# Kernel tuning notes

Measured on AMD Instinct MI355X. Metric: run time of the kernel, lower is better.

Reference implementation:

```python
import jax, jax.numpy as jnp
import numpy as np

TOKENS, HIDDEN, FFN = 4096, 4096, 14336
SCALE = 0.02  # keep activations in a sane range


def setup_inputs() -> dict:
    key = jax.random.key(0)
    k1, k2, k3, k4 = jax.random.split(key, 4)
    x = jax.random.normal(k1, (TOKENS, HIDDEN), dtype=jnp.float32)
    expert_w1 = jax.random.normal(k2, (FFN, HIDDEN), dtype=jnp.float32) * SCALE
    expert_v1 = jax.random.normal(k3, (FFN, HIDDEN), dtype=jnp.float32) * SCALE
    expert_w2 = jax.random.normal(k4, (FFN, HIDDEN), dtype=jnp.float32) * SCALE
    return {"x": x, "expert_w1": expert_w1, "expert_v1": expert_v1, "expert_w2": expert_w2}


def reference(x, expert_w1, expert_v1, expert_w2):
    # gate/up projections: [T, H] @ [H, F] -> [T, F]
    gate = jnp.einsum('th,fh->tf', x, expert_w1)
    up = jnp.einsum('th,fh->tf', x, expert_v1)
    inter = jax.nn.silu(gate) * up            # fused SwiGLU intermediate [T, F]
    down = jnp.einsum('tf,fh->th', inter, expert_w2)  # [T, H]
    return down
```

## Files before the change

### kernel.cpp

```cpp
#include <hip/hip_runtime.h>
#include <hip/hip_bf16.h>
#include <stdint.h>

#define TOKENS 4096
#define HIDDEN 4096
#define FFN    14336

typedef __attribute__((ext_vector_type(8))) short bf16x8;
typedef __attribute__((ext_vector_type(4))) float f32x4;
typedef __attribute__((ext_vector_type(8))) unsigned short u16x8;

typedef __attribute__((address_space(3))) void lds_void_t;
typedef const __attribute__((address_space(1))) void gbl_void_t;

static __device__ __forceinline__ unsigned short f2b(float f) {
  union { float f; unsigned int u; } v; v.f = f;
  unsigned int u = v.u;
  return (unsigned short)((u + 0x7FFFu + ((u >> 16) & 1u)) >> 16);
}

__global__ void cvt_kernel(const float* __restrict__ in, unsigned short* __restrict__ out, long n) {
  long idx = (long)blockIdx.x * blockDim.x + threadIdx.x;
  long stride = (long)gridDim.x * blockDim.x;
  for (long i = idx * 4; i < n; i += stride * 4) {
    const float4 v = *reinterpret_cast<const float4*>(in + i);
    ushort4 o;
    o.x = f2b(v.x); o.y = f2b(v.y); o.z = f2b(v.z); o.w = f2b(v.w);
    *reinterpret_cast<ushort4*>(out + i) = o;
  }
}

__global__ void transpose_cvt_kernel(const float* __restrict__ in, unsigned short* __restrict__ out) {
  __shared__ float tile[64][65];
  const int f0 = blockIdx.x * 64;
  const int h0 = blockIdx.y * 64;
  const int t = threadIdx.x;
  const int rcol = (t & 15) * 4;
  const int rrow = t >> 4;
#pragma unroll
  for (int it = 0; it < 4; ++it) {
    int r = rrow + it * 16;
    const float4 v = *reinterpret_cast<const float4*>(in + (long)(f0 + r) * HIDDEN + h0 + rcol);
    tile[r][rcol] = v.x; tile[r][rcol + 1] = v.y; tile[r][rcol + 2] = v.z; tile[r][rcol + 3] = v.w;
  }
  __syncthreads();
  const int wrow = t >> 2;
  const int wc = (t & 3) * 16;
  u16x8 lo, hi;
#pragma unroll
  for (int j = 0; j < 8; ++j) lo[j] = f2b(tile[wc + j][wrow]);
#pragma unroll
  for (int j = 0; j < 8; ++j) hi[j] = f2b(tile[wc + 8 + j][wrow]);
  u16x8* dst = reinterpret_cast<u16x8*>(out + (long)(h0 + wrow) * FFN + f0 + wc);
  dst[0] = lo; dst[1] = hi;
}

#define MFMA16(a, b, c) __builtin_amdgcn_mfma_f32_16x16x32_bf16((a), (b), (c), 0, 0, 0)
#define SBAR()  __builtin_amdgcn_s_barrier()

static __device__ __forceinline__ int xcd_chunk(int bid, int nwg) {
  return (bid & 7) * (nwg >> 3) + (bid >> 3);
}

__global__ __launch_bounds__(512, 2)
void gateup256p_kernel(const unsigned short* __restrict__ X,
                       const unsigned short* __restrict__ W1,
                       const unsigned short* __restrict__ V1,
                       unsigned short* __restrict__ Inter) {
  __shared__ unsigned short sh[65536];
  const int tid = threadIdx.x, lane = tid & 63, wid = tid >> 6;
  const int wm = wid >> 2, wn = wid & 3;
  const int p = blockIdx.x;
  const int bm = p & 15;
  const int bnl = p >> 4;
  const int sr = tid >> 3;
  const int scb = (((tid & 7) ^ (sr & 7)) << 4);
  const int l15 = lane & 15;
  const int cb0 = (((lane >> 4) * 16) ^ ((lane & 7) << 4));
  const int cb1 = ((64 + (lane >> 4) * 16) ^ ((lane & 7) << 4));

  const unsigned short* Ap = X + (long)(bm * 256) * HIDDEN;

  auto LDA8 = [&](bf16x8* a, int buf, int cb) {
    const char* base = (const char*)sh + buf * 65536 + wm * 16384 + l15 * 128 + cb;
#pragma unroll
    for (int m = 0; m < 8; ++m) a[m] = *(const bf16x8*)(base + m * 2048);
  };
  auto LDW2 = [&](bf16x8* w, int buf, int cb) {
    const char* base = (const char*)sh + buf * 65536 + 32768 + (wn * 32 + l15) * 128 + cb;
    w[0] = *(const bf16x8*)(base);
    w[1] = *(const bf16x8*)(base + 2048);
  };
  auto LDV2 = [&](bf16x8* v, int buf, int cb) {
    const char* base = (const char*)sh + buf * 65536 + 49152 + (wn * 32 + l15) * 128 + cb;
    v[0] = *(const bf16x8*)(base);
    v[1] = *(const bf16x8*)(base + 2048);
  };

  for (int j = 0; j < 7; ++j) {
    const int bn = j * 16 + bnl;
    const unsigned short* Wp = W1 + (long)(bn * 128) * HIDDEN;
    const unsigned short* Vp = V1 + (long)(bn * 128) * HIDDEN;

    auto STA = [&](int u, int buf, int t) {
      const unsigned short* src = Ap + (long)(u * 64 + sr) * HIDDEN + t * 64 + (scb >> 1);
      unsigned short* dst = sh + buf * 32768 + u * 4096 + tid * 8;
      __builtin_amdgcn_global_load_lds((gbl_void_t*)src, (lds_void_t*)dst, 16, 0, 0);
    };
    auto STW = [&](int u, int buf, int t) {
      const unsigned short* src = Wp + (long)(u * 64 + sr) * HIDDEN + t * 64 + (scb >> 1);
      unsigned short* dst = sh + buf * 32768 + 16384 + u * 4096 + tid * 8;
      __builtin_amdgcn_global_load_lds((gbl_void_t*)src, (lds_void_t*)dst, 16, 0, 0);
    };
    auto STV = [&](int u, int buf, int t) {
      const unsigned short* src = Vp + (long)(u * 64 + sr) * HIDDEN + t * 64 + (scb >> 1);
      unsigned short* dst = sh + buf * 32768 + 24576 + u * 4096 + tid * 8;
      __builtin_amdgcn_global_load_lds((gbl_void_t*)src, (lds_void_t*)dst, 16, 0, 0);
    };

    f32x4 accg[8][2] = {};
    f32x4 accu[8][2] = {};

    STA(0, 0, 0); STA(1, 0, 0); STA(2, 0, 0); STA(3, 0, 0);
    STW(0, 0, 0); STW(1, 0, 0); STV(0, 0, 0); STV(1, 0, 0);

    bf16x8 a[8], w[2], v[2];
    const int NT = HIDDEN / 64;
    for (int t = 0; t < NT; ++t) {
      const int cur = t & 1, nxt = cur ^ 1;
      const bool pre = (t + 1 < NT);
      if (pre) { STW(0, nxt, t + 1); STW(1, nxt, t + 1);
                 STV(0, nxt, t + 1); STV(1, nxt, t + 1);
                 asm volatile("s_waitcnt vmcnt(4)" ::: "memory"); }
      else     { asm volatile("s_waitcnt vmcnt(0)" ::: "memory"); }
      SBAR();
      LDA8(a, cur, cb0); LDW2(w, cur, cb0);
      __builtin_amdgcn_s_setprio(1);
#pragma unroll
      for (int m = 0; m < 8; ++m) {
        accg[m][0] = MFMA16(a[m], w[0], accg[m][0]);
        accg[m][1] = MFMA16(a[m], w[1], accg[m][1]);
      }
      __builtin_amdgcn_s_setprio(0);
      SBAR();
      if (pre) { STA(0, nxt, t + 1); STA(1, nxt, t + 1);
                 STA(2, nxt, t + 1); STA(3, nxt, t + 1); }
      LDV2(v, cur, cb0);
      __builtin_amdgcn_s_setprio(1);
#pragma unroll
      for (int m = 0; m < 8; ++m) {
        accu[m][0] = MFMA16(a[m], v[0], accu[m][0]);
        accu[m][1] = MFMA16(a[m], v[1], accu[m][1]);
      }
      __builtin_amdgcn_s_setprio(0);
      SBAR();
      LDA8(a, cur, cb1); LDW2(w, cur, cb1);
      __builtin_amdgcn_s_setprio(1);
#pragma unroll
      for (int m = 0; m < 8; ++m) {
        accg[m][0] = MFMA16(a[m], w[0], accg[m][0]);
        accg[m][1] = MFMA16(a[m], w[1], accg[m][1]);
      }
      __builtin_amdgcn_s_setprio(0);
      SBAR();
      LDV2(v, cur, cb1);
      __builtin_amdgcn_s_setprio(1);
#pragma unroll
      for (int m = 0; m < 8; ++m) {
        accu[m][0] = MFMA16(a[m], v[0], accu[m][0]);
        accu[m][1] = MFMA16(a[m], v[1], accu[m][1]);
      }
      __builtin_amdgcn_s_setprio(0);
      SBAR();
    }
    const int r0 = (lane >> 4) * 4;
#pragma unroll
    for (int m = 0; m < 8; ++m)
#pragma unroll
      for (int n = 0; n < 2; ++n)
#pragma unroll
        for (int r = 0; r < 4; ++r) {
          const float g = accg[m][n][r];
          const float u = accu[m][n][r];
          const float s = g / (1.0f + __expf(-g));
          const int row = bm * 256 + wm * 128 + m * 16 + r0 + r;
          const int col = bn * 128 + wn * 32 + n * 16 + l15;
          Inter[(long)row * FFN + col] = f2b(s * u);
        }
    asm volatile("s_waitcnt vmcnt(0)" ::: "memory");
  }
}

__global__ __launch_bounds__(512, 2)
void down256_kernel(const unsigned short* __restrict__ Inter,
                    const unsigned short* __restrict__ W2t,
                    float* __restrict__ Out) {
  __shared__ unsigned short sh[65536];
  const int tid = threadIdx.x, lane = tid & 63, wid = tid >> 6;
  const int wm = wid >> 2, wn = wid & 3;
  const int swz = xcd_chunk(blockIdx.x, (TOKENS / 256) * (HIDDEN / 256));
  const int bm = swz & 15;
  const int bn = swz >> 4;
  const int sr = tid >> 3;
  const int scb = (((tid & 7) ^ (sr & 7)) << 4);
  const int l15 = lane & 15;
  const int cb0 = (((lane >> 4) * 16) ^ ((lane & 7) << 4));
  const int cb1 = ((64 + (lane >> 4) * 16) ^ ((lane & 7) << 4));

  const unsigned short* Ap = Inter + (long)(bm * 256) * FFN;
  const unsigned short* Bp = W2t + (long)(bn * 256) * FFN;

  f32x4 acc[8][4] = {};

  auto STAGE = [&](int kind, int h, int buf, int t) {
    const unsigned short* src = (kind ? Bp : Ap) + (long)(h * 128 + sr) * FFN + t * 64 + (scb >> 1);
    unsigned short* dst = sh + buf * 32768 + kind * 16384 + h * 8192 + tid * 8;
    __builtin_amdgcn_global_load_lds((gbl_void_t*)src, (lds_void_t*)dst, 16, 0, 0);
    __builtin_amdgcn_global_load_lds((gbl_void_t*)(src + 64L * FFN), (lds_void_t*)(dst + 4096), 16, 0, 0);
  };
  auto LDA8 = [&](bf16x8* a, int buf, int cb) {
    const char* base = (const char*)sh + buf * 65536 + wm * 16384 + l15 * 128 + cb;
#pragma unroll
    for (int m = 0; m < 8; ++m) a[m] = *(const bf16x8*)(base + m * 2048);
  };
  auto LDB2 = [&](bf16x8* b, int buf, int cb, int np) {
    const char* base = (const char*)sh + buf * 65536 + 32768 + (wn >> 1) * 16384 +
                       ((wn & 1) * 64 + l15) * 128 + cb;
    b[2 * np]     = *(const bf16x8*)(base + (2 * np) * 2048);
    b[2 * np + 1] = *(const bf16x8*)(base + (2 * np + 1) * 2048);
  };

  STAGE(0, 0, 0, 0); STAGE(0, 1, 0, 0); STAGE(1, 0, 0, 0); STAGE(1, 1, 0, 0);

  bf16x8 a[8], b[4];
  const int NT = FFN / 64;
  for (int t = 0; t < NT; ++t) {
    const int cur = t & 1, nxt = cur ^ 1;
    const bool pre = (t + 1 < NT);
    if (pre) { STAGE(1, 0, nxt, t + 1); STAGE(1, 1, nxt, t + 1);
               asm volatile("s_waitcnt vmcnt(4)" ::: "memory"); }
    else     { asm volatile("s_waitcnt vmcnt(0)" ::: "memory"); }
    SBAR();
    LDA8(a, cur, cb0); LDB2(b, cur, cb0, 0);
    __builtin_amdgcn_s_setprio(1);
#pragma unroll
    for (int m = 0; m < 8; ++m) {
      acc[m][0] = MFMA16(a[m], b[0], acc[m][0]);
      acc[m][1] = MFMA16(a[m], b[1], acc[m][1]);
    }
    __builtin_amdgcn_s_setprio(0);
    SBAR();
    if (pre) { STAGE(0, 0, nxt, t + 1); STAGE(0, 1, nxt, t + 1); }
    LDB2(b, cur, cb0, 1);
    __builtin_amdgcn_s_setprio(1);
#pragma unroll
    for (int m = 0; m < 8; ++m) {
      acc[m][2] = MFMA16(a[m], b[2], acc[m][2]);
      acc[m][3] = MFMA16(a[m], b[3], acc[m][3]);
    }
    __builtin_amdgcn_s_setprio(0);
    SBAR();
    LDA8(a, cur, cb1); LDB2(b, cur, cb1, 0);
    __builtin_amdgcn_s_setprio(1);
#pragma unroll
    for (int m = 0; m < 8; ++m) {
      acc[m][0] = MFMA16(a[m], b[0], acc[m][0]);
      acc[m][1] = MFMA16(a[m], b[1], acc[m][1]);
    }
    __builtin_amdgcn_s_setprio(0);
    SBAR();
    LDB2(b, cur, cb1, 1);
    __builtin_amdgcn_s_setprio(1);
#pragma unroll
    for (int m = 0; m < 8; ++m) {
      acc[m][2] = MFMA16(a[m], b[2], acc[m][2]);
      acc[m][3] = MFMA16(a[m], b[3], acc[m][3]);
    }
    __builtin_amdgcn_s_setprio(0);
    SBAR();
  }
  const int r0 = (lane >> 4) * 4;
#pragma unroll
  for (int m = 0; m < 8; ++m)
#pragma unroll
    for (int n = 0; n < 4; ++n)
#pragma unroll
      for (int r = 0; r < 4; ++r) {
        const int row = bm * 256 + wm * 128 + m * 16 + r0 + r;
        const int col = bn * 256 + wn * 64 + n * 16 + l15;
        Out[(long)row * HIDDEN + col] = acc[m][n][r];
      }
}

__device__ __forceinline__ void stage_tile_128(const unsigned short* __restrict__ g, long ldk,
                                               unsigned short* lds, int wave, int lane) {
#pragma unroll
  for (int it = 0; it < 2; ++it) {
    const int row = (it * 4 + wave) * 16 + (lane >> 2);
    const int kcol = (lane & 3) * 8;
    const unsigned short* src = g + (long)row * ldk + kcol;
    unsigned short* dst = lds + row * 32 + kcol;
    __builtin_amdgcn_global_load_lds((gbl_void_t*)src, (lds_void_t*)dst, 16, 0, 0);
  }
}

__global__ __launch_bounds__(256, 2)
void down_nt_kernel(const unsigned short* __restrict__ Inter,
                    const float* __restrict__ W2,
                    float* __restrict__ Out) {
  __shared__ unsigned short As[128 * 32];
  __shared__ unsigned short Bs[128 * 32];
  const int t = threadIdx.x;
  const int lane = t & 63;
  const int wave = t >> 6;
  const int bm = blockIdx.x & 31;
  const int bn = blockIdx.x >> 5;
  const int wm = (wave >> 1) * 64;
  const int wn = (wave & 1) * 64;
  const unsigned short* gA = Inter + (long)(bm * 128) * FFN;

  f32x4 acc[4][4] = {};
  const int fr = lane & 15;
  const int kg = (lane >> 4) * 8;
  const int p = lane & 15;
  const int h0 = wave * 32 + (lane >> 4) * 8;
  const float* gB = W2 + bn * 128 + h0;

  for (int kt = 0; kt < FFN; kt += 32) {
    __syncthreads();
    stage_tile_128(gA + kt, FFN, As, wave, lane);
    const float* r0p = gB + (long)(kt + 2 * p) * HIDDEN;
    const float* r1p = r0p + HIDDEN;
    const float4 a0 = *reinterpret_cast<const float4*>(r0p);
    const float4 a1 = *reinterpret_cast<const float4*>(r0p + 4);
    const float4 b0 = *reinterpret_cast<const float4*>(r1p);
    const float4 b1 = *reinterpret_cast<const float4*>(r1p + 4);
    unsigned short lo[8], hi[8];
    lo[0] = f2b(a0.x); lo[1] = f2b(a0.y); lo[2] = f2b(a0.z); lo[3] = f2b(a0.w);
    lo[4] = f2b(a1.x); lo[5] = f2b(a1.y); lo[6] = f2b(a1.z); lo[7] = f2b(a1.w);
    hi[0] = f2b(b0.x); hi[1] = f2b(b0.y); hi[2] = f2b(b0.z); hi[3] = f2b(b0.w);
    hi[4] = f2b(b1.x); hi[5] = f2b(b1.y); hi[6] = f2b(b1.z); hi[7] = f2b(b1.w);
#pragma unroll
    for (int j = 0; j < 8; ++j) {
      const unsigned int pack = (unsigned int)lo[j] | ((unsigned int)hi[j] << 16);
      *reinterpret_cast<unsigned int*>(&Bs[(h0 + j) * 32 + 2 * p]) = pack;
    }
    __syncthreads();
    bf16x8 a[4], b[4];
#pragma unroll
    for (int m = 0; m < 4; ++m)
      a[m] = *reinterpret_cast<const bf16x8*>(&As[(wm + m * 16 + fr) * 32 + kg]);
#pragma unroll
    for (int n = 0; n < 4; ++n)
      b[n] = *reinterpret_cast<const bf16x8*>(&Bs[(wn + n * 16 + fr) * 32 + kg]);
#pragma unroll
    for (int m = 0; m < 4; ++m)
#pragma unroll
      for (int n = 0; n < 4; ++n)
        acc[m][n] = MFMA16(a[m], b[n], acc[m][n]);
  }
  const int r0 = (lane >> 4) * 4;
#pragma unroll
  for (int m = 0; m < 4; ++m)
#pragma unroll
    for (int n = 0; n < 4; ++n)
#pragma unroll
      for (int r = 0; r < 4; ++r) {
        const int row = bm * 128 + wm + m * 16 + r0 + r;
        const int col = bn * 128 + wn + n * 16 + fr;
        Out[(long)row * HIDDEN + col] = acc[m][n][r];
      }
}

extern "C" void kernel_launch(void* const* d_in, const int* in_sizes, int n_in,
                              void* d_out, int out_size, void* d_ws, size_t ws_size,
                              hipStream_t stream) {
  const float* x  = (const float*)d_in[0];
  const float* w1 = (const float*)d_in[1];
  const float* v1 = (const float*)d_in[2];
  const float* w2 = (const float*)d_in[3];
  float* out = (float*)d_out;

  const size_t REQ_SMALL = 385875968UL;
  const size_t REQ_FULL  = 503316480UL;
  if (ws_size < REQ_SMALL) return;
  const bool full = (ws_size >= REQ_FULL);
  char* ws = (char*)d_ws;
  unsigned short* xb     = (unsigned short*)(ws);
  unsigned short* w1b    = (unsigned short*)(ws + 33554432L);
  unsigned short* v1b    = (unsigned short*)(ws + 150994944L);
  unsigned short* interb = (unsigned short*)(ws + 268435456L);
  unsigned short* w2tb   = (unsigned short*)(ws + 385875968L);

  hipLaunchKernelGGL(cvt_kernel, dim3(2048), dim3(256), 0, stream, x,  xb,  (long)TOKENS * HIDDEN);
  hipLaunchKernelGGL(cvt_kernel, dim3(2048), dim3(256), 0, stream, w1, w1b, (long)FFN * HIDDEN);
  hipLaunchKernelGGL(cvt_kernel, dim3(2048), dim3(256), 0, stream, v1, v1b, (long)FFN * HIDDEN);
  if (full)
    hipLaunchKernelGGL(transpose_cvt_kernel, dim3(FFN / 64, HIDDEN / 64), dim3(256), 0, stream, w2, w2tb);
  hipLaunchKernelGGL(gateup256p_kernel, dim3(256), dim3(512), 0, stream,
                     xb, w1b, v1b, interb);
  if (full)
    hipLaunchKernelGGL(down256_kernel, dim3((TOKENS / 256) * (HIDDEN / 256)), dim3(512), 0, stream,
                       interb, w2tb, out);
  else
    hipLaunchKernelGGL(down_nt_kernel, dim3((TOKENS / 128) * (HIDDEN / 128)), dim3(256), 0, stream,
                       interb, w2, out);
}
```

Measured before the change: 1.434 ms.

## Switch gate/up and down GEMMs from 16x16x32 to 32x32x16 MFMA tiles

Replaces the 16x16x32 bf16 MFMA instructions in both the fused gate/up kernel and the down-projection kernel with 32x32x16 MFMAs. It reworks the LDS fragment loads, swizzled addressing and accumulator layout (f32x16 per 32x32 tile), and remaps the epilogue row and column indexing. Larger MFMA tiles cut the number of LDS fragment reads per FLOP and the instruction issue count. The trade-off is longer dependent MFMA chains on each accumulator and a new epilogue layout that must match the 32x32 output mapping.

```diff
diff --git a/kernel.cpp b/kernel.cpp
--- a/kernel.cpp
+++ b/kernel.cpp
@@ -8,6 +8,7 @@
 
 typedef __attribute__((ext_vector_type(8))) short bf16x8;
 typedef __attribute__((ext_vector_type(4))) float f32x4;
+typedef __attribute__((ext_vector_type(16))) float f32x16;
 typedef __attribute__((ext_vector_type(8))) unsigned short u16x8;
 
 typedef __attribute__((address_space(3))) void lds_void_t;
@@ -55,6 +56,7 @@
   dst[0] = lo; dst[1] = hi;
 }
 
+#define MFMA32(a, b, c) __builtin_amdgcn_mfma_f32_32x32x16_bf16((a), (b), (c), 0, 0, 0)
 #define MFMA16(a, b, c) __builtin_amdgcn_mfma_f32_16x16x32_bf16((a), (b), (c), 0, 0, 0)
 #define SBAR()  __builtin_amdgcn_s_barrier()
 
@@ -75,26 +77,24 @@
   const int bnl = p >> 4;
   const int sr = tid >> 3;
   const int scb = (((tid & 7) ^ (sr & 7)) << 4);
-  const int l15 = lane & 15;
-  const int cb0 = (((lane >> 4) * 16) ^ ((lane & 7) << 4));
-  const int cb1 = ((64 + (lane >> 4) * 16) ^ ((lane & 7) << 4));
+  const int l31 = lane & 31;
+  const int kb16 = (lane >> 5) * 16;
+  const int swz = (lane & 7) << 4;
 
   const unsigned short* Ap = X + (long)(bm * 256) * HIDDEN;
 
-  auto LDA8 = [&](bf16x8* a, int buf, int cb) {
-    const char* base = (const char*)sh + buf * 65536 + wm * 16384 + l15 * 128 + cb;
-#pragma unroll
-    for (int m = 0; m < 8; ++m) a[m] = *(const bf16x8*)(base + m * 2048);
-  };
-  auto LDW2 = [&](bf16x8* w, int buf, int cb) {
-    const char* base = (const char*)sh + buf * 65536 + 32768 + (wn * 32 + l15) * 128 + cb;
-    w[0] = *(const bf16x8*)(base);
-    w[1] = *(const bf16x8*)(base + 2048);
-  };
-  auto LDV2 = [&](bf16x8* v, int buf, int cb) {
-    const char* base = (const char*)sh + buf * 65536 + 49152 + (wn * 32 + l15) * 128 + cb;
-    v[0] = *(const bf16x8*)(base);
-    v[1] = *(const bf16x8*)(base + 2048);
+  auto LDA4 = [&](bf16x8* a, int buf, int kb) {
+    const char* base = (const char*)sh + buf * 65536 + (wm * 128 + l31) * 128 + ((kb + kb16) ^ swz);
+#pragma unroll
+    for (int rt = 0; rt < 4; ++rt) a[rt] = *(const bf16x8*)(base + rt * 32 * 128);
+  };
+  auto LDW1 = [&](bf16x8& w, int buf, int kb) {
+    const char* base = (const char*)sh + buf * 65536 + 32768 + (wn * 32 + l31) * 128 + ((kb + kb16) ^ swz);
+    w = *(const bf16x8*)(base);
+  };
+  auto LDV1 = [&](bf16x8& v, int buf, int kb) {
+    const char* base = (const char*)sh + buf * 65536 + 49152 + (wn * 32 + l31) * 128 + ((kb + kb16) ^ swz);
+    v = *(const bf16x8*)(base);
   };
 
   for (int j = 0; j < 7; ++j) {
@@ -118,13 +118,13 @@
       __builtin_amdgcn_global_load_lds((gbl_void_t*)src, (lds_void_t*)dst, 16, 0, 0);
     };
 
-    f32x4 accg[8][2] = {};
-    f32x4 accu[8][2] = {};
+    f32x16 accg[4] = {};
+    f32x16 accu[4] = {};
 
     STA(0, 0, 0); STA(1, 0, 0); STA(2, 0, 0); STA(3, 0, 0);
     STW(0, 0, 0); STW(1, 0, 0); STV(0, 0, 0); STV(1, 0, 0);
 
-    bf16x8 a[8], w[2], v[2];
+    bf16x8 a0[4], a1[4], w0, w1, v0, v1;
     const int NT = HIDDEN / 64;
     for (int t = 0; t < NT; ++t) {
       const int cur = t & 1, nxt = cur ^ 1;
@@ -134,59 +134,58 @@
                  asm volatile("s_waitcnt vmcnt(4)" ::: "memory"); }
       else     { asm volatile("s_waitcnt vmcnt(0)" ::: "memory"); }
       SBAR();
-      LDA8(a, cur, cb0); LDW2(w, cur, cb0);
+      LDA4(a0, cur, 0); LDA4(a1, cur, 32); LDW1(w0, cur, 0); LDW1(w1, cur, 32);
       __builtin_amdgcn_s_setprio(1);
 #pragma unroll
-      for (int m = 0; m < 8; ++m) {
-        accg[m][0] = MFMA16(a[m], w[0], accg[m][0]);
-        accg[m][1] = MFMA16(a[m], w[1], accg[m][1]);
+      for (int rt = 0; rt < 4; ++rt) {
+        accg[rt] = MFMA32(a0[rt], w0, accg[rt]);
+        accg[rt] = MFMA32(a1[rt], w1, accg[rt]);
       }
       __builtin_amdgcn_s_setprio(0);
       SBAR();
       if (pre) { STA(0, nxt, t + 1); STA(1, nxt, t + 1);
                  STA(2, nxt, t + 1); STA(3, nxt, t + 1); }
-      LDV2(v, cur, cb0);
+      LDV1(v0, cur, 0); LDV1(v1, cur, 32);
       __builtin_amdgcn_s_setprio(1);
 #pragma unroll
-      for (int m = 0; m < 8; ++m) {
-        accu[m][0] = MFMA16(a[m], v[0], accu[m][0]);
-        accu[m][1] = MFMA16(a[m], v[1], accu[m][1]);
+      for (int rt = 0; rt < 4; ++rt) {
+        accu[rt] = MFMA32(a0[rt], v0, accu[rt]);
+        accu[rt] = MFMA32(a1[rt], v1, accu[rt]);
       }
       __builtin_amdgcn_s_setprio(0);
       SBAR();
-      LDA8(a, cur, cb1); LDW2(w, cur, cb1);
+      LDA4(a0, cur, 64); LDA4(a1, cur, 96); LDW1(w0, cur, 64); LDW1(w1, cur, 96);
       __builtin_amdgcn_s_setprio(1);
 #pragma unroll
-      for (int m = 0; m < 8; ++m) {
-        accg[m][0] = MFMA16(a[m], w[0], accg[m][0]);
-        accg[m][1] = MFMA16(a[m], w[1], accg[m][1]);
+      for (int rt = 0; rt < 4; ++rt) {
+        accg[rt] = MFMA32(a0[rt], w0, accg[rt]);
+        accg[rt] = MFMA32(a1[rt], w1, accg[rt]);
       }
       __builtin_amdgcn_s_setprio(0);
       SBAR();
-      LDV2(v, cur, cb1);
+      LDV1(v0, cur, 64); LDV1(v1, cur, 96);
       __builtin_amdgcn_s_setprio(1);
 #pragma unroll
-      for (int m = 0; m < 8; ++m) {
-        accu[m][0] = MFMA16(a[m], v[0], accu[m][0]);
-        accu[m][1] = MFMA16(a[m], v[1], accu[m][1]);
+      for (int rt = 0; rt < 4; ++rt) {
+        accu[rt] = MFMA32(a0[rt], v0, accu[rt]);
+        accu[rt] = MFMA32(a1[rt], v1, accu[rt]);
       }
       __builtin_amdgcn_s_setprio(0);
       SBAR();
     }
-    const int r0 = (lane >> 4) * 4;
-#pragma unroll
-    for (int m = 0; m < 8; ++m)
-#pragma unroll
-      for (int n = 0; n < 2; ++n)
-#pragma unroll
-        for (int r = 0; r < 4; ++r) {
-          const float g = accg[m][n][r];
-          const float u = accu[m][n][r];
-          const float s = g / (1.0f + __expf(-g));
-          const int row = bm * 256 + wm * 128 + m * 16 + r0 + r;
-          const int col = bn * 128 + wn * 32 + n * 16 + l15;
-          Inter[(long)row * FFN + col] = f2b(s * u);
-        }
+    const int rbase = 4 * (lane >> 5);
+    const int col = bn * 128 + wn * 32 + l31;
+#pragma unroll
+    for (int rt = 0; rt < 4; ++rt)
+#pragma unroll
+      for (int r = 0; r < 16; ++r) {
+        const int grow = (r & 3) + 8 * (r >> 2) + rbase;
+        const int row = bm * 256 + wm * 128 + rt * 32 + grow;
+        const float g = accg[rt][r];
+        const float u = accu[rt][r];
+        const float s = g / (1.0f + __expf(-g));
+        Inter[(long)row * FFN + col] = f2b(s * u);
+      }
     asm volatile("s_waitcnt vmcnt(0)" ::: "memory");
   }
 }
@@ -198,19 +197,19 @@
   __shared__ unsigned short sh[65536];
   const int tid = threadIdx.x, lane = tid & 63, wid = tid >> 6;
   const int wm = wid >> 2, wn = wid & 3;
-  const int swz = xcd_chunk(blockIdx.x, (TOKENS / 256) * (HIDDEN / 256));
-  const int bm = swz & 15;
-  const int bn = swz >> 4;
+  const int swz2 = xcd_chunk(blockIdx.x, (TOKENS / 256) * (HIDDEN / 256));
+  const int bm = swz2 & 15;
+  const int bn = swz2 >> 4;
   const int sr = tid >> 3;
   const int scb = (((tid & 7) ^ (sr & 7)) << 4);
-  const int l15 = lane & 15;
-  const int cb0 = (((lane >> 4) * 16) ^ ((lane & 7) << 4));
-  const int cb1 = ((64 + (lane >> 4) * 16) ^ ((lane & 7) << 4));
+  const int l31 = lane & 31;
+  const int kb16 = (lane >> 5) * 16;
+  const int swz = (lane & 7) << 4;
 
   const unsigned short* Ap = Inter + (long)(bm * 256) * FFN;
   const unsigned short* Bp = W2t + (long)(bn * 256) * FFN;
 
-  f32x4 acc[8][4] = {};
+  f32x16 acc[4][2] = {};
 
   auto STAGE = [&](int kind, int h, int buf, int t) {
     const unsigned short* src = (kind ? Bp : Ap) + (long)(h * 128 + sr) * FFN + t * 64 + (scb >> 1);
@@ -218,21 +217,21 @@
     __builtin_amdgcn_global_load_lds((gbl_void_t*)src, (lds_void_t*)dst, 16, 0, 0);
     __builtin_amdgcn_global_load_lds((gbl_void_t*)(src + 64L * FFN), (lds_void_t*)(dst + 4096), 16, 0, 0);
   };
-  auto LDA8 = [&](bf16x8* a, int buf, int cb) {
-    const char* base = (const char*)sh + buf * 65536 + wm * 16384 + l15 * 128 + cb;
-#pragma unroll
-    for (int m = 0; m < 8; ++m) a[m] = *(const bf16x8*)(base + m * 2048);
-  };
-  auto LDB2 = [&](bf16x8* b, int buf, int cb, int np) {
-    const char* base = (const char*)sh + buf * 65536 + 32768 + (wn >> 1) * 16384 +
-                       ((wn & 1) * 64 + l15) * 128 + cb;
-    b[2 * np]     = *(const bf16x8*)(base + (2 * np) * 2048);
-    b[2 * np + 1] = *(const bf16x8*)(base + (2 * np + 1) * 2048);
+  auto LDA4 = [&](bf16x8* a, int buf, int kb) {
+    const char* base = (const char*)sh + buf * 65536 + (wm * 128 + l31) * 128 + ((kb + kb16) ^ swz);
+#pragma unroll
+    for (int rt = 0; rt < 4; ++rt) a[rt] = *(const bf16x8*)(base + rt * 32 * 128);
+  };
+  auto LDB1 = [&](bf16x8& b, int buf, int ct, int kb) {
+    const int hrow = wn * 64 + ct * 32 + l31;
+    const char* base = (const char*)sh + buf * 65536 + 32768 + (hrow >> 7) * 16384 +
+                       (hrow & 127) * 128 + ((kb + kb16) ^ swz);
+    b = *(const bf16x8*)(base);
   };
 
   STAGE(0, 0, 0, 0); STAGE(0, 1, 0, 0); STAGE(1, 0, 0, 0); STAGE(1, 1, 0, 0);
 
-  bf16x8 a[8], b[4];
+  bf16x8 a0[4], a1[4], b0, b1;
   const int NT = FFN / 64;
   for (int t = 0; t < NT; ++t) {
     const int cur = t & 1, nxt = cur ^ 1;
@@ -241,55 +240,57 @@
                asm volatile("s_waitcnt vmcnt(4)" ::: "memory"); }
     else     { asm volatile("s_waitcnt vmcnt(0)" ::: "memory"); }
     SBAR();
-    LDA8(a, cur, cb0); LDB2(b, cur, cb0, 0);
+    LDA4(a0, cur, 0); LDA4(a1, cur, 32); LDB1(b0, cur, 0, 0); LDB1(b1, cur, 0, 32);
     __builtin_amdgcn_s_setprio(1);
 #pragma unroll
-    for (int m = 0; m < 8; ++m) {
-      acc[m][0] = MFMA16(a[m], b[0], acc[m][0]);
-      acc[m][1] = MFMA16(a[m], b[1], acc[m][1]);
+    for (int rt = 0; rt < 4; ++rt) {
+      acc[rt][0] = MFMA32(a0[rt], b0, acc[rt][0]);
+      acc[rt][0] = MFMA32(a1[rt], b1, acc[rt][0]);
     }
     __builtin_amdgcn_s_setprio(0);
     SBAR();
     if (pre) { STAGE(0, 0, nxt, t + 1); STAGE(0, 1, nxt, t + 1); }
-    LDB2(b, cur, cb0, 1);
+    LDB1(b0, cur, 1, 0); LDB1(b1, cur, 1, 32);
     __builtin_amdgcn_s_setprio(1);
 #pragma unroll
-    for (int m = 0; m < 8; ++m) {
-      acc[m][2] = MFMA16(a[m], b[2], acc[m][2]);
-      acc[m][3] = MFMA16(a[m], b[3], acc[m][3]);
+    for (int rt = 0; rt < 4; ++rt) {
+      acc[rt][1] = MFMA32(a0[rt], b0, acc[rt][1]);
+      acc[rt][1] = MFMA32(a1[rt], b1, acc[rt][1]);
     }
     __builtin_amdgcn_s_setprio(0);
     SBAR();
-    LDA8(a, cur, cb1); LDB2(b, cur, cb1, 0);
+    LDA4(a0, cur, 64); LDA4(a1, cur, 96); LDB1(b0, cur, 0, 64); LDB1(b1, cur, 0, 96);
     __builtin_amdgcn_s_setprio(1);
 #pragma unroll
-    for (int m = 0; m < 8; ++m) {
-      acc[m][0] = MFMA16(a[m], b[0], acc[m][0]);
-      acc[m][1] = MFMA16(a[m], b[1], acc[m][1]);
+    for (int rt = 0; rt < 4; ++rt) {
+      acc[rt][0] = MFMA32(a0[rt], b0, acc[rt][0]);
+      acc[rt][0] = MFMA32(a1[rt], b1, acc[rt][0]);
     }
     __builtin_amdgcn_s_setprio(0);
     SBAR();
-    LDB2(b, cur, cb1, 1);
+    LDB1(b0, cur, 1, 64); LDB1(b1, cur, 1, 96);
     __builtin_amdgcn_s_setprio(1);
 #pragma unroll
-    for (int m = 0; m < 8; ++m) {
-      acc[m][2] = MFMA16(a[m], b[2], acc[m][2]);
-      acc[m][3] = MFMA16(a[m], b[3], acc[m][3]);
+    for (int rt = 0; rt < 4; ++rt) {
+      acc[rt][1] = MFMA32(a0[rt], b0, acc[rt][1]);
+      acc[rt][1] = MFMA32(a1[rt], b1, acc[rt][1]);
     }
     __builtin_amdgcn_s_setprio(0);
     SBAR();
   }
-  const int r0 = (lane >> 4) * 4;
-#pragma unroll
-  for (int m = 0; m < 8; ++m)
-#pragma unroll
-    for (int n = 0; n < 4; ++n)
-#pragma unroll
-      for (int r = 0; r < 4; ++r) {
-        const int row = bm * 256 + wm * 128 + m * 16 + r0 + r;
-        const int col = bn * 256 + wn * 64 + n * 16 + l15;
-        Out[(long)row * HIDDEN + col] = acc[m][n][r];
-      }
+  const int rbase = 4 * (lane >> 5);
+#pragma unroll
+  for (int rt = 0; rt < 4; ++rt)
+#pragma unroll
+    for (int ct = 0; ct < 2; ++ct) {
+      const int col = bn * 256 + wn * 64 + ct * 32 + l31;
+#pragma unroll
+      for (int r = 0; r < 16; ++r) {
+        const int grow = (r & 3) + 8 * (r >> 2) + rbase;
+        const int row = bm * 256 + wm * 128 + rt * 32 + grow;
+        Out[(long)row * HIDDEN + col] = acc[rt][ct][r];
+      }
+    }
 }
 
 __device__ __forceinline__ void stage_tile_128(const unsigned short* __restrict__ g, long ldk,
```

After: 1.603 ms. +11.8%, slower.

## Triple-buffer W1/V1 tiles and prefetch two k-steps ahead in gate/up GEMM

Applied to the files above, without the earlier changes.

Splits LDS into a double-buffered X region and a triple-buffered W1/V1 region. Weight tiles are now issued two iterations ahead, and the X loads for the next step move to right after the top barrier. The goal is to hide more global-load latency behind the MFMA work. LDS use grows to 160 KB per block, which may limit occupancy or fail to fit if the budget is smaller.

```diff
diff --git a/kernel.cpp b/kernel.cpp
--- a/kernel.cpp
+++ b/kernel.cpp
@@ -67,7 +67,7 @@
                        const unsigned short* __restrict__ W1,
                        const unsigned short* __restrict__ V1,
                        unsigned short* __restrict__ Inter) {
-  __shared__ unsigned short sh[65536];
+  __shared__ unsigned short sh[81920];
   const int tid = threadIdx.x, lane = tid & 63, wid = tid >> 6;
   const int wm = wid >> 2, wn = wid & 3;
   const int p = blockIdx.x;
@@ -81,18 +81,18 @@
 
   const unsigned short* Ap = X + (long)(bm * 256) * HIDDEN;
 
-  auto LDA8 = [&](bf16x8* a, int buf, int cb) {
-    const char* base = (const char*)sh + buf * 65536 + wm * 16384 + l15 * 128 + cb;
+  auto LDA8 = [&](bf16x8* a, int bufA, int cb) {
+    const char* base = (const char*)sh + bufA * 32768 + wm * 16384 + l15 * 128 + cb;
 #pragma unroll
     for (int m = 0; m < 8; ++m) a[m] = *(const bf16x8*)(base + m * 2048);
   };
-  auto LDW2 = [&](bf16x8* w, int buf, int cb) {
-    const char* base = (const char*)sh + buf * 65536 + 32768 + (wn * 32 + l15) * 128 + cb;
+  auto LDW2 = [&](bf16x8* w, int b3, int cb) {
+    const char* base = (const char*)sh + 65536 + b3 * 32768 + (wn * 32 + l15) * 128 + cb;
     w[0] = *(const bf16x8*)(base);
     w[1] = *(const bf16x8*)(base + 2048);
   };
-  auto LDV2 = [&](bf16x8* v, int buf, int cb) {
-    const char* base = (const char*)sh + buf * 65536 + 49152 + (wn * 32 + l15) * 128 + cb;
+  auto LDV2 = [&](bf16x8* v, int b3, int cb) {
+    const char* base = (const char*)sh + 65536 + b3 * 32768 + 16384 + (wn * 32 + l15) * 128 + cb;
     v[0] = *(const bf16x8*)(base);
     v[1] = *(const bf16x8*)(base + 2048);
   };
@@ -102,39 +102,40 @@
     const unsigned short* Wp = W1 + (long)(bn * 128) * HIDDEN;
     const unsigned short* Vp = V1 + (long)(bn * 128) * HIDDEN;
 
-    auto STA = [&](int u, int buf, int t) {
+    auto STA = [&](int u, int bufA, int t) {
       const unsigned short* src = Ap + (long)(u * 64 + sr) * HIDDEN + t * 64 + (scb >> 1);
-      unsigned short* dst = sh + buf * 32768 + u * 4096 + tid * 8;
+      unsigned short* dst = sh + bufA * 16384 + u * 4096 + tid * 8;
       __builtin_amdgcn_global_load_lds((gbl_void_t*)src, (lds_void_t*)dst, 16, 0, 0);
     };
-    auto STW = [&](int u, int buf, int t) {
+    auto STW = [&](int u, int b3, int t) {
       const unsigned short* src = Wp + (long)(u * 64 + sr) * HIDDEN + t * 64 + (scb >> 1);
-      unsigned short* dst = sh + buf * 32768 + 16384 + u * 4096 + tid * 8;
+      unsigned short* dst = sh + 32768 + b3 * 16384 + u * 4096 + tid * 8;
       __builtin_amdgcn_global_load_lds((gbl_void_t*)src, (lds_void_t*)dst, 16, 0, 0);
     };
-    auto STV = [&](int u, int buf, int t) {
+    auto STV = [&](int u, int b3, int t) {
       const unsigned short* src = Vp + (long)(u * 64 + sr) * HIDDEN + t * 64 + (scb >> 1);
-      unsigned short* dst = sh + buf * 32768 + 24576 + u * 4096 + tid * 8;
+      unsigned short* dst = sh + 32768 + b3 * 16384 + 8192 + u * 4096 + tid * 8;
       __builtin_amdgcn_global_load_lds((gbl_void_t*)src, (lds_void_t*)dst, 16, 0, 0);
     };
 
     f32x4 accg[8][2] = {};
     f32x4 accu[8][2] = {};
 
+    STW(0, 0, 0); STW(1, 0, 0); STV(0, 0, 0); STV(1, 0, 0);
     STA(0, 0, 0); STA(1, 0, 0); STA(2, 0, 0); STA(3, 0, 0);
-    STW(0, 0, 0); STW(1, 0, 0); STV(0, 0, 0); STV(1, 0, 0);
+    STW(0, 1, 1); STW(1, 1, 1); STV(0, 1, 1); STV(1, 1, 1);
 
     bf16x8 a[8], w[2], v[2];
     const int NT = HIDDEN / 64;
     for (int t = 0; t < NT; ++t) {
-      const int cur = t & 1, nxt = cur ^ 1;
-      const bool pre = (t + 1 < NT);
-      if (pre) { STW(0, nxt, t + 1); STW(1, nxt, t + 1);
-                 STV(0, nxt, t + 1); STV(1, nxt, t + 1);
-                 asm volatile("s_waitcnt vmcnt(4)" ::: "memory"); }
-      else     { asm volatile("s_waitcnt vmcnt(0)" ::: "memory"); }
+      const int curA = t & 1, nxtA = curA ^ 1;
+      const int b3 = t % 3, b3w = (t + 2) % 3;
+      if (t + 1 < NT) { asm volatile("s_waitcnt vmcnt(4)" ::: "memory"); }
+      else            { asm volatile("s_waitcnt vmcnt(0)" ::: "memory"); }
       SBAR();
-      LDA8(a, cur, cb0); LDW2(w, cur, cb0);
+      if (t + 1 < NT) { STA(0, nxtA, t + 1); STA(1, nxtA, t + 1);
+                        STA(2, nxtA, t + 1); STA(3, nxtA, t + 1); }
+      LDA8(a, curA, cb0); LDW2(w, b3, cb0);
       __builtin_amdgcn_s_setprio(1);
 #pragma unroll
       for (int m = 0; m < 8; ++m) {
@@ -143,9 +144,9 @@
       }
       __builtin_amdgcn_s_setprio(0);
       SBAR();
-      if (pre) { STA(0, nxt, t + 1); STA(1, nxt, t + 1);
-                 STA(2, nxt, t + 1); STA(3, nxt, t + 1); }
-      LDV2(v, cur, cb0);
+      if (t + 2 < NT) { STW(0, b3w, t + 2); STW(1, b3w, t + 2);
+                        STV(0, b3w, t + 2); STV(1, b3w, t + 2); }
+      LDV2(v, b3, cb0);
       __builtin_amdgcn_s_setprio(1);
 #pragma unroll
       for (int m = 0; m < 8; ++m) {
@@ -154,7 +155,7 @@
       }
       __builtin_amdgcn_s_setprio(0);
       SBAR();
-      LDA8(a, cur, cb1); LDW2(w, cur, cb1);
+      LDA8(a, curA, cb1); LDW2(w, b3, cb1);
       __builtin_amdgcn_s_setprio(1);
 #pragma unroll
       for (int m = 0; m < 8; ++m) {
@@ -163,7 +164,7 @@
       }
       __builtin_amdgcn_s_setprio(0);
       SBAR();
-      LDV2(v, cur, cb1);
+      LDV2(v, b3, cb1);
       __builtin_amdgcn_s_setprio(1);
 #pragma unroll
       for (int m = 0; m < 8; ++m) {
```

New measurement: 1.412 ms. Within noise of the previous version (-1.5%).
